# Kernel optimization log

Hardware: AMD Instinct MI355X
Metric: run time of the kernel (lower is better)

Reference implementation:

```python
import jax, jax.numpy as jnp
import numpy as np

B, T, E = 2, 2048, 1024
H = 16
DH = E // H  # 64
DFF = 4 * E
EPS = 1e-5


def _layernorm(x, gamma, beta):
    mu = jnp.mean(x, axis=-1, keepdims=True)
    var = jnp.mean((x - mu) ** 2, axis=-1, keepdims=True)
    return (x - mu) * jax.lax.rsqrt(var + EPS) * gamma + beta


def setup_inputs() -> dict:
    key = jax.random.key(0)
    ks = jax.random.split(key, 16)
    s_e = 1.0 / np.sqrt(E)
    s_f = 1.0 / np.sqrt(DFF)
    return {
        "x": jax.random.normal(ks[0], (B, T, E), jnp.float32),
        # per-head QKV projections, stacked over heads [H, E, DH]
        "Wq": jax.random.normal(ks[1], (H, E, DH), jnp.float32) * s_e,
        "bq": jnp.zeros((H, DH), jnp.float32),
        "Wk": jax.random.normal(ks[2], (H, E, DH), jnp.float32) * s_e,
        "bk": jnp.zeros((H, DH), jnp.float32),
        "Wv": jax.random.normal(ks[3], (H, E, DH), jnp.float32) * s_e,
        "bv": jnp.zeros((H, DH), jnp.float32),
        # output projection
        "Wo": jax.random.normal(ks[4], (E, E), jnp.float32) * s_e,
        "bo": jnp.zeros((E,), jnp.float32),
        # feed-forward
        "W1": jax.random.normal(ks[5], (E, DFF), jnp.float32) * s_e,
        "b1": jnp.zeros((DFF,), jnp.float32),
        "W2": jax.random.normal(ks[6], (DFF, E), jnp.float32) * s_f,
        "b2": jnp.zeros((E,), jnp.float32),
        # layernorms
        "gamma1": jnp.ones((E,), jnp.float32),
        "beta1": jnp.zeros((E,), jnp.float32),
        "gamma2": jnp.ones((E,), jnp.float32),
        "beta2": jnp.zeros((E,), jnp.float32),
    }


def reference(x, Wq, bq, Wk, bk, Wv, bv, Wo, bo, W1, b1, W2, b2,
              gamma1, beta1, gamma2, beta2):
    Bc, Tc, Ec = x.shape
    # --- multi-head causal self-attention (dropout = eval/identity) ---
    xn = _layernorm(x, gamma1, beta1)
    q = jnp.einsum('bte,hed->bhtd', xn, Wq) + bq[:, None, :]
    k = jnp.einsum('bte,hed->bhtd', xn, Wk) + bk[:, None, :]
    v = jnp.einsum('bte,hed->bhtd', xn, Wv) + bv[:, None, :]
    scale = 1.0 / np.sqrt(q.shape[-1])
    scores = jnp.einsum('bhtd,bhsd->bhts', q, k) * scale  # [B,H,T,T]
    causal = jnp.tril(jnp.ones((Tc, Tc), bool))
    scores = jnp.where(causal, scores, jnp.float32(-1e9))
    attn = jax.nn.softmax(scores, axis=-1)
    out = jnp.einsum('bhts,bhsd->bhtd', attn, v)          # [B,H,T,DH]
    out = out.transpose(0, 2, 1, 3).reshape(Bc, Tc, Ec)    # concat heads
    out = out @ Wo + bo
    x = x + out
    # --- feed-forward ---
    xn2 = _layernorm(x, gamma2, beta2)
    h = jax.nn.relu(xn2 @ W1 + b1)
    x = x + (h @ W2 + b2)
    return x
```

## Files before the change

kernel.cpp:

```cpp
#include <hip/hip_runtime.h>
#include <stdint.h>

#define BT    4096
#define EDIM  1024
#define TLEN  2048
#define NH    16
#define DHH   64
#define DFFN  4096

typedef short short8 __attribute__((ext_vector_type(8)));
typedef float f32x4  __attribute__((ext_vector_type(4)));

__device__ __forceinline__ float bf2f(unsigned short u) {
    union { unsigned int i; float f; } c; c.i = ((unsigned int)u) << 16; return c.f;
}
__device__ __forceinline__ unsigned short f2bf(float f) {
    union { float f; unsigned int i; } c; c.f = f;
    unsigned int u = c.i;
    unsigned int r = u + 0x7fffu + ((u >> 16) & 1u);
    return (unsigned short)(r >> 16);
}
__device__ __forceinline__ float fexp2(float x) {
#if __has_builtin(__builtin_amdgcn_exp2f)
    return __builtin_amdgcn_exp2f(x);
#else
    return __expf(x * 0.69314718056f);
#endif
}

template<int QKV>
__global__ __launch_bounds__(256) void transpose_kernel(
    const float* src, unsigned short* dst, int Kdim, int srcStride)
{
    __shared__ float T[64][65];
    int t = threadIdx.x;
    int n0 = blockIdx.x * 64, k0 = blockIdx.y * 64;
    int r = t >> 4, c4 = (t & 15) * 4;
    #pragma unroll
    for (int i = 0; i < 4; i++) {
        int rr = r + i * 16;
        const float* p;
        if (QKV) p = src + ((size_t)(n0 >> 6)) * 65536 + (size_t)(k0 + rr) * 64 + c4;
        else     p = src + (size_t)(k0 + rr) * srcStride + n0 + c4;
        float4 v = *(const float4*)p;
        T[c4 + 0][rr] = v.x;
        T[c4 + 1][rr] = v.y;
        T[c4 + 2][rr] = v.z;
        T[c4 + 3][rr] = v.w;
    }
    __syncthreads();
    int rn = t >> 2, ck = (t & 3) * 16;
    short8 o0, o1;
    #pragma unroll
    for (int j = 0; j < 8; j++) o0[j] = (short)f2bf(T[rn][ck + j]);
    #pragma unroll
    for (int j = 0; j < 8; j++) o1[j] = (short)f2bf(T[rn][ck + 8 + j]);
    unsigned short* dp = dst + (size_t)(n0 + rn) * Kdim + k0 + ck;
    *(short8*)dp       = o0;
    *(short8*)(dp + 8) = o1;
}

__global__ __launch_bounds__(256) void vtrans_kernel(
    const unsigned short* __restrict__ v, unsigned short* __restrict__ vt)
{
    __shared__ __align__(16) unsigned short T[64][72];
    int bh = blockIdx.x, st = blockIdx.y;
    int t = threadIdx.x;
    int r = t >> 2, c = (t & 3) * 16;
    const unsigned short* src = v + ((size_t)bh * TLEN + st * 64) * DHH;
    short8 a0 = *(const short8*)(src + r * DHH + c);
    short8 a1 = *(const short8*)(src + r * DHH + c + 8);
    *(short8*)&T[r][c]     = a0;
    *(short8*)&T[r][c + 8] = a1;
    __syncthreads();
    int d = t >> 2;
    short8 o0, o1;
    #pragma unroll
    for (int j = 0; j < 8; j++) o0[j] = (short)T[c + j][d];
    #pragma unroll
    for (int j = 0; j < 8; j++) o1[j] = (short)T[c + 8 + j][d];
    unsigned short* dst = vt + ((size_t)bh * DHH + d) * TLEN + st * 64 + c;
    *(short8*)dst       = o0;
    *(short8*)(dst + 8) = o1;
}

template<int F32IN>
__global__ __launch_bounds__(256) void ln_stats_kernel(
    const void* __restrict__ x, float* __restrict__ mu_out, float* __restrict__ rstd_out)
{
    int row = blockIdx.x, tid = threadIdx.x;
    size_t off = (size_t)row * EDIM + tid * 4;
    float v0, v1, v2, v3;
    if (F32IN) {
        float4 a = *(const float4*)((const float*)x + off);
        v0 = a.x; v1 = a.y; v2 = a.z; v3 = a.w;
    } else {
        ushort4 raw = *(const ushort4*)((const unsigned short*)x + off);
        v0 = bf2f(raw.x); v1 = bf2f(raw.y); v2 = bf2f(raw.z); v3 = bf2f(raw.w);
    }
    float s  = v0 + v1 + v2 + v3;
    float ss = v0*v0 + v1*v1 + v2*v2 + v3*v3;
    #pragma unroll
    for (int o = 1; o < 64; o <<= 1) {
        s  += __shfl_xor(s,  o, 64);
        ss += __shfl_xor(ss, o, 64);
    }
    __shared__ float red[8];
    int wave = tid >> 6;
    if ((tid & 63) == 0) { red[wave*2] = s; red[wave*2+1] = ss; }
    __syncthreads();
    if (tid == 0) {
        s  = red[0] + red[2] + red[4] + red[6];
        ss = red[1] + red[3] + red[5] + red[7];
        float mu  = s * (1.0f / EDIM);
        float var = ss * (1.0f / EDIM) - mu * mu;
        mu_out[row]   = mu;
        rstd_out[row] = rsqrtf(var + 1e-5f);
    }
}

template<int F32IN>
__global__ __launch_bounds__(256) void ln_apply_kernel(
    const void* __restrict__ x, const float* __restrict__ mu, const float* __restrict__ rstd,
    const float* __restrict__ g, const float* __restrict__ b, unsigned short* __restrict__ out)
{
    int row = blockIdx.x, tid = threadIdx.x;
    float m = mu[row], rs = rstd[row];
    size_t off = (size_t)row * EDIM + tid * 4;
    float v0, v1, v2, v3;
    if (F32IN) {
        float4 a = *(const float4*)((const float*)x + off);
        v0 = a.x; v1 = a.y; v2 = a.z; v3 = a.w;
    } else {
        ushort4 raw = *(const ushort4*)((const unsigned short*)x + off);
        v0 = bf2f(raw.x); v1 = bf2f(raw.y); v2 = bf2f(raw.z); v3 = bf2f(raw.w);
    }
    float4 gv = *(const float4*)(g + tid * 4);
    float4 bv = *(const float4*)(b + tid * 4);
    ushort4 o;
    o.x = f2bf((v0 - m) * rs * gv.x + bv.x);
    o.y = f2bf((v1 - m) * rs * gv.y + bv.y);
    o.z = f2bf((v2 - m) * rs * gv.z + bv.z);
    o.w = f2bf((v3 - m) * rs * gv.w + bv.w);
    *(ushort4*)(out + off) = o;
}

#define V_QKV  0
#define V_WO   1
#define V_FF1  2
#define V_FF2A 3
#define V_FF2B 4
#define LDKK 72

template<int VARIANT, int BN>
__global__ __launch_bounds__(256) void gemm_bt_kernel(
    const unsigned short* A,
    const unsigned short* Bt,
    const float* bias,
    const void* resid,
    void* out,
    int N, int K)
{
    constexpr int NJ = BN / 32;
    __shared__ __align__(16) unsigned short As[128 * LDKK];
    __shared__ __align__(16) unsigned short Bs[BN * LDKK];
    int tid  = threadIdx.x;
    int lane = tid & 63, wave = tid >> 6;
    int quad = lane >> 4, l16 = lane & 15;
    int wr = wave >> 1, wc = wave & 1;
    int m0 = blockIdx.y * 128, n0 = blockIdx.x * BN;

    f32x4 acc[4][NJ];
    #pragma unroll
    for (int i = 0; i < 4; i++)
        #pragma unroll
        for (int j = 0; j < NJ; j++) acc[i][j] = (f32x4){0.f, 0.f, 0.f, 0.f};

    int rowA = tid >> 1, colA = (tid & 1) * 32;
    int rowB, colB;
    if (BN == 128) { rowB = tid >> 1; colB = (tid & 1) * 32; }
    else           { rowB = tid >> 2; colB = (tid & 3) * 16; }

    for (int k0 = 0; k0 < K; k0 += 64) {
        const unsigned short* ap = A + (size_t)(m0 + rowA) * K + k0 + colA;
        short8 a0 = *(const short8*)ap;
        short8 a1 = *(const short8*)(ap + 8);
        short8 a2 = *(const short8*)(ap + 16);
        short8 a3 = *(const short8*)(ap + 24);
        const unsigned short* bp = Bt + (size_t)(n0 + rowB) * K + k0 + colB;
        short8 b0 = *(const short8*)bp;
        short8 b1 = *(const short8*)(bp + 8);
        short8 b2, b3;
        if (BN == 128) {
            b2 = *(const short8*)(bp + 16);
            b3 = *(const short8*)(bp + 24);
        }

        *(short8*)(&As[rowA * LDKK + colA])      = a0;
        *(short8*)(&As[rowA * LDKK + colA + 8])  = a1;
        *(short8*)(&As[rowA * LDKK + colA + 16]) = a2;
        *(short8*)(&As[rowA * LDKK + colA + 24]) = a3;
        *(short8*)(&Bs[rowB * LDKK + colB])      = b0;
        *(short8*)(&Bs[rowB * LDKK + colB + 8])  = b1;
        if (BN == 128) {
            *(short8*)(&Bs[rowB * LDKK + colB + 16]) = b2;
            *(short8*)(&Bs[rowB * LDKK + colB + 24]) = b3;
        }

        __syncthreads();

        #pragma unroll
        for (int ks = 0; ks < 2; ks++) {
            short8 af[4], bf[NJ];
            #pragma unroll
            for (int i = 0; i < 4; i++)
                af[i] = *(const short8*)(&As[(wr * 64 + i * 16 + l16) * LDKK + ks * 32 + quad * 8]);
            #pragma unroll
            for (int j = 0; j < NJ; j++)
                bf[j] = *(const short8*)(&Bs[(wc * (BN / 2) + j * 16 + l16) * LDKK + ks * 32 + quad * 8]);
            #pragma unroll
            for (int i = 0; i < 4; i++)
                #pragma unroll
                for (int j = 0; j < NJ; j++)
                    acc[i][j] = __builtin_amdgcn_mfma_f32_16x16x32_bf16(af[i], bf[j], acc[i][j], 0, 0, 0);
        }

        __syncthreads();
    }

    #pragma unroll
    for (int j = 0; j < NJ; j++) {
        int c = n0 + wc * (BN / 2) + j * 16 + l16;
        float bi = (VARIANT == V_FF2A) ? 0.0f : bias[c];
        #pragma unroll
        for (int i = 0; i < 4; i++) {
            #pragma unroll
            for (int r = 0; r < 4; r++) {
                int m = m0 + wr * 64 + i * 16 + quad * 4 + r;
                float val = acc[i][j][r] + bi;
                if (VARIANT == V_WO)
                    val += ((const float*)resid)[(size_t)m * N + c];
                if (VARIANT == V_FF2B)
                    val += bf2f(((const unsigned short*)resid)[(size_t)m * N + c])
                         + ((const float*)out)[(size_t)m * N + c];
                if (VARIANT == V_FF1)
                    val = fmaxf(val, 0.0f);
                if (VARIANT == V_QKV) {
                    int b = m >> 11, t = m & 2047, h = c >> 6, d = c & 63;
                    ((unsigned short*)out)[(((size_t)(b * NH + h)) * TLEN + t) * DHH + d] = f2bf(val);
                } else if (VARIANT == V_FF2A || VARIANT == V_FF2B) {
                    ((float*)out)[(size_t)m * N + c] = val;
                } else {
                    ((unsigned short*)out)[(size_t)m * N + c] = f2bf(val);
                }
            }
        }
    }
}

__global__ __launch_bounds__(256) void attn_kernel(
    const unsigned short* __restrict__ q,
    const unsigned short* __restrict__ k,
    const unsigned short* __restrict__ vt,
    unsigned short* __restrict__ att)
{
    __shared__ __align__(16) unsigned short Ks[128 * 72];
    __shared__ __align__(16) unsigned short Vs[64 * 136];
    __shared__ __align__(16) unsigned short Ps[4][16 * 136];
    int tid  = threadIdx.x;
    int lane = tid & 63, wave = tid >> 6;
    int quad = lane >> 4, l16 = lane & 15;

    int flat = blockIdx.x;
    int xcd  = flat & 7, idx = flat >> 3;
    int bh   = xcd * 4 + (idx >> 5);
    int qt   = 31 - (idx & 31);
    int q0   = qt * 64;
    int qw   = q0 + wave * 16;

    const unsigned short* Qb = q  + ((size_t)bh * TLEN + qw) * DHH;
    const unsigned short* Kb = k  + (size_t)bh * TLEN * DHH;
    const unsigned short* Vb = vt + (size_t)bh * DHH * TLEN;

    short8 aq0 = *(const short8*)(Qb + l16 * DHH + quad * 8);
    short8 aq1 = *(const short8*)(Qb + l16 * DHH + 32 + quad * 8);

    f32x4 o[4];
    #pragma unroll
    for (int n = 0; n < 4; n++) o[n] = (f32x4){0.f, 0.f, 0.f, 0.f};
    f32x4 mrow = {-1e30f, -1e30f, -1e30f, -1e30f};
    f32x4 lrow = {0.f, 0.f, 0.f, 0.f};
    unsigned short* Pw = Ps[wave];
    const float cs = 0.18033688011f;

    int rowK = tid >> 1, colK = (tid & 1) * 32;
    int rowV = tid >> 2, colV = (tid & 3) * 32;

    int nch = (q0 >> 7) + 1;

    short8 ka0, ka1, ka2, ka3, va0, va1, va2, va3;
    {
        const unsigned short* kp = Kb + (size_t)rowK * DHH + colK;
        ka0 = *(const short8*)kp;
        ka1 = *(const short8*)(kp + 8);
        ka2 = *(const short8*)(kp + 16);
        ka3 = *(const short8*)(kp + 24);
        const unsigned short* vp = Vb + (size_t)rowV * TLEN + colV;
        va0 = *(const short8*)vp;
        va1 = *(const short8*)(vp + 8);
        va2 = *(const short8*)(vp + 16);
        va3 = *(const short8*)(vp + 24);
    }

    for (int ch = 0; ch < nch; ch++) {
        int s0 = ch * 128;
        __syncthreads();
        *(short8*)(&Ks[rowK * 72 + colK])       = ka0;
        *(short8*)(&Ks[rowK * 72 + colK + 8])   = ka1;
        *(short8*)(&Ks[rowK * 72 + colK + 16])  = ka2;
        *(short8*)(&Ks[rowK * 72 + colK + 24])  = ka3;
        *(short8*)(&Vs[rowV * 136 + colV])      = va0;
        *(short8*)(&Vs[rowV * 136 + colV + 8])  = va1;
        *(short8*)(&Vs[rowV * 136 + colV + 16]) = va2;
        *(short8*)(&Vs[rowV * 136 + colV + 24]) = va3;
        __syncthreads();

        if (ch + 1 < nch) {
            int s1 = s0 + 128;
            const unsigned short* kp = Kb + (size_t)(s1 + rowK) * DHH + colK;
            ka0 = *(const short8*)kp;
            ka1 = *(const short8*)(kp + 8);
            ka2 = *(const short8*)(kp + 16);
            ka3 = *(const short8*)(kp + 24);
            const unsigned short* vp = Vb + (size_t)rowV * TLEN + s1 + colV;
            va0 = *(const short8*)vp;
            va1 = *(const short8*)(vp + 8);
            va2 = *(const short8*)(vp + 16);
            va3 = *(const short8*)(vp + 24);
        }

        f32x4 S[8];
        #pragma unroll
        for (int n = 0; n < 8; n++) {
            short8 b0 = *(const short8*)(&Ks[(n * 16 + l16) * 72 + quad * 8]);
            short8 b1 = *(const short8*)(&Ks[(n * 16 + l16) * 72 + 32 + quad * 8]);
            f32x4 s = (f32x4){0.f, 0.f, 0.f, 0.f};
            s = __builtin_amdgcn_mfma_f32_16x16x32_bf16(aq0, b0, s, 0, 0, 0);
            s = __builtin_amdgcn_mfma_f32_16x16x32_bf16(aq1, b1, s, 0, 0, 0);
            S[n] = s;
        }
        bool needmask = (s0 + 127 > qw);
        #pragma unroll
        for (int r = 0; r < 4; r++) {
            float xv[8];
            #pragma unroll
            for (int n = 0; n < 8; n++) {
                float xx = S[n][r] * cs;
                if (needmask && (s0 + n * 16 + l16 > qw + quad * 4 + r)) xx = -1e30f;
                xv[n] = xx;
            }
            float mx = fmaxf(fmaxf(fmaxf(xv[0], xv[1]), fmaxf(xv[2], xv[3])),
                             fmaxf(fmaxf(xv[4], xv[5]), fmaxf(xv[6], xv[7])));
            mx = fmaxf(mx, __shfl_xor(mx, 1, 64));
            mx = fmaxf(mx, __shfl_xor(mx, 2, 64));
            mx = fmaxf(mx, __shfl_xor(mx, 4, 64));
            mx = fmaxf(mx, __shfl_xor(mx, 8, 64));
            float used;
            if (__all(mx <= mrow[r] + 8.0f)) {
                used = mrow[r];
            } else {
                float mnew  = fmaxf(mrow[r], mx);
                float alpha = fexp2(mrow[r] - mnew);
                lrow[r] *= alpha;
                o[0][r] *= alpha; o[1][r] *= alpha;
                o[2][r] *= alpha; o[3][r] *= alpha;
                mrow[r] = mnew;
                used = mnew;
            }
            float ps = 0.f;
            int prow = (quad * 4 + r) * 136;
            #pragma unroll
            for (int n = 0; n < 8; n++) {
                float p = fexp2(xv[n] - used);
                ps += p;
                Pw[prow + n * 16 + l16] = f2bf(p);
            }
            lrow[r] += ps;
        }
        short8 ap[4];
        #pragma unroll
        for (int ks = 0; ks < 4; ks++)
            ap[ks] = *(const short8*)(Pw + l16 * 136 + ks * 32 + quad * 8);
        #pragma unroll
        for (int n = 0; n < 4; n++) {
            #pragma unroll
            for (int ks = 0; ks < 4; ks++) {
                short8 b = *(const short8*)(&Vs[(n * 16 + l16) * 136 + ks * 32 + quad * 8]);
                o[n] = __builtin_amdgcn_mfma_f32_16x16x32_bf16(ap[ks], b, o[n], 0, 0, 0);
            }
        }
    }

    int bidx = bh >> 4, hh = bh & 15;
    #pragma unroll
    for (int r = 0; r < 4; r++) {
        float ls = lrow[r];
        ls += __shfl_xor(ls, 1, 64);
        ls += __shfl_xor(ls, 2, 64);
        ls += __shfl_xor(ls, 4, 64);
        ls += __shfl_xor(ls, 8, 64);
        float inv = 1.0f / ls;
        int t = qw + quad * 4 + r;
        size_t rowoff = ((size_t)(bidx * TLEN + t)) * EDIM + hh * 64;
        #pragma unroll
        for (int n = 0; n < 4; n++)
            att[rowoff + n * 16 + l16] = f2bf(o[n][r] * inv);
    }
}

extern "C" void kernel_launch(void* const* d_in, const int* in_sizes, int n_in,
                              void* d_out, int out_size, void* d_ws, size_t ws_size,
                              hipStream_t stream)
{
    (void)in_sizes; (void)n_in; (void)out_size; (void)ws_size;
    const float* x   = (const float*)d_in[0];
    const float* Wq  = (const float*)d_in[1];
    const float* bq  = (const float*)d_in[2];
    const float* Wk  = (const float*)d_in[3];
    const float* bk  = (const float*)d_in[4];
    const float* Wv  = (const float*)d_in[5];
    const float* bv  = (const float*)d_in[6];
    const float* Wo  = (const float*)d_in[7];
    const float* bo  = (const float*)d_in[8];
    const float* W1  = (const float*)d_in[9];
    const float* b1  = (const float*)d_in[10];
    const float* W2  = (const float*)d_in[11];
    const float* b2  = (const float*)d_in[12];
    const float* g1  = (const float*)d_in[13];
    const float* be1 = (const float*)d_in[14];
    const float* g2  = (const float*)d_in[15];
    const float* be2 = (const float*)d_in[16];

    unsigned short* ws  = (unsigned short*)d_ws;
    unsigned short* xn  = ws;
    unsigned short* vtg = ws;
    unsigned short* qb  = ws + 4194304;
    unsigned short* kb  = ws + 8388608;
    unsigned short* vb  = ws + 12582912;
    unsigned short* wqt = ws + 16777216;
    unsigned short* wkt = ws + 17825792;
    unsigned short* wvt = ws + 18874368;
    unsigned short* att = ws + 16777216;
    unsigned short* x1  = ws + 4194304;
    unsigned short* wot = ws + 8388608;
    unsigned short* w1t = ws + 8388608;
    unsigned short* w2t = ws + 10485760;
    unsigned short* hb  = ws + 12582912;
    float* mu1 = (float*)((char*)d_ws + 41943040);
    float* rs1 = mu1 + 4096;
    float* mu2 = mu1 + 8192;
    float* rs2 = mu1 + 12288;

    dim3 gT64(16, 16);
    dim3 gE(EDIM / 64, BT / 128);
    dim3 gF(2048 / 128, BT / 128);

    transpose_kernel<1><<<gT64, 256, 0, stream>>>(Wq, wqt, EDIM, 64);
    transpose_kernel<1><<<gT64, 256, 0, stream>>>(Wk, wkt, EDIM, 64);
    transpose_kernel<1><<<gT64, 256, 0, stream>>>(Wv, wvt, EDIM, 64);

    ln_stats_kernel<1><<<BT, 256, 0, stream>>>(x, mu1, rs1);
    ln_apply_kernel<1><<<BT, 256, 0, stream>>>(x, mu1, rs1, g1, be1, xn);

    gemm_bt_kernel<V_QKV, 64><<<gE, 256, 0, stream>>>(xn, wqt, bq, nullptr, qb, EDIM, EDIM);
    gemm_bt_kernel<V_QKV, 64><<<gE, 256, 0, stream>>>(xn, wkt, bk, nullptr, kb, EDIM, EDIM);
    gemm_bt_kernel<V_QKV, 64><<<gE, 256, 0, stream>>>(xn, wvt, bv, nullptr, vb, EDIM, EDIM);

    vtrans_kernel<<<dim3(NH * 2, TLEN / 64), 256, 0, stream>>>(vb, vtg);

    attn_kernel<<<dim3(1024), 256, 0, stream>>>(qb, kb, vtg, att);

    transpose_kernel<0><<<gT64, 256, 0, stream>>>(Wo, wot, EDIM, EDIM);
    gemm_bt_kernel<V_WO, 64><<<gE, 256, 0, stream>>>(att, wot, bo, x, x1, EDIM, EDIM);

    ln_stats_kernel<0><<<BT, 256, 0, stream>>>(x1, mu2, rs2);
    ln_apply_kernel<0><<<BT, 256, 0, stream>>>(x1, mu2, rs2, g2, be2, xn);

    transpose_kernel<0><<<dim3(32, 16), 256, 0, stream>>>(W1, w1t, EDIM, DFFN);
    transpose_kernel<0><<<dim3(16, 32), 256, 0, stream>>>(W2, w2t, 2048, EDIM);
    gemm_bt_kernel<V_FF1, 128><<<gF, 256, 0, stream>>>(xn, w1t, b1, nullptr, hb, 2048, EDIM);
    gemm_bt_kernel<V_FF2A, 64><<<gE, 256, 0, stream>>>(hb, w2t, nullptr, nullptr, d_out, EDIM, 2048);
    transpose_kernel<0><<<dim3(32, 16), 256, 0, stream>>>(W1 + 2048, w1t, EDIM, DFFN);
    transpose_kernel<0><<<dim3(16, 32), 256, 0, stream>>>(W2 + (size_t)2048 * EDIM, w2t, 2048, EDIM);
    gemm_bt_kernel<V_FF1, 128><<<gF, 256, 0, stream>>>(xn, w1t, b1 + 2048, nullptr, hb, 2048, EDIM);
    gemm_bt_kernel<V_FF2B, 64><<<gE, 256, 0, stream>>>(hb, w2t, b2, x1, d_out, EDIM, 2048);
}
```

Measured before the change: 463.7 us.

## Use direct global-to-LDS loads in GEMM and fuse Q/K/V projections into one launch

GEMM tile loads now use the global_load_lds builtin, which writes 16-byte chunks straight into unpadded shared memory instead of going through registers. The Q, K and V weight transposes are written contiguously and their biases packed into one buffer, so a single GEMM with N=3072 replaces three launches. The aim is to cut register staging and launch overhead and to fill the GPU better with a larger grid. Dropping the LDS padding can bring back bank conflicts on the MFMA fragment reads.

```diff
diff --git a/kernel.cpp b/kernel.cpp
--- a/kernel.cpp
+++ b/kernel.cpp
@@ -11,6 +11,9 @@
 typedef short short8 __attribute__((ext_vector_type(8)));
 typedef float f32x4  __attribute__((ext_vector_type(4)));
 
+typedef const __attribute__((address_space(1))) unsigned int* gas_ptr;
+typedef __attribute__((address_space(3))) unsigned int*       las_ptr;
+
 __device__ __forceinline__ float bf2f(unsigned short u) {
     union { unsigned int i; float f; } c; c.i = ((unsigned int)u) << 16; return c.f;
 }
@@ -26,6 +29,9 @@
 #else
     return __expf(x * 0.69314718056f);
 #endif
+}
+__device__ __forceinline__ void gload16(const unsigned short* g, unsigned short* l) {
+    __builtin_amdgcn_global_load_lds((gas_ptr)g, (las_ptr)l, 16, 0, 0);
 }
 
 template<int QKV>
@@ -84,6 +90,15 @@
     *(short8*)(dst + 8) = o1;
 }
 
+__global__ __launch_bounds__(256) void bias_fuse_kernel(
+    const float* __restrict__ bq, const float* __restrict__ bk,
+    const float* __restrict__ bv, float* __restrict__ dst)
+{
+    int t = blockIdx.x * 256 + threadIdx.x;
+    const float* src = (t < 1024) ? bq : (t < 2048) ? bk : bv;
+    dst[t] = src[t & 1023];
+}
+
 template<int F32IN>
 __global__ __launch_bounds__(256) void ln_stats_kernel(
     const void* __restrict__ x, float* __restrict__ mu_out, float* __restrict__ rstd_out)
@@ -150,7 +165,6 @@
 #define V_FF1  2
 #define V_FF2A 3
 #define V_FF2B 4
-#define LDKK 72
 
 template<int VARIANT, int BN>
 __global__ __launch_bounds__(256) void gemm_bt_kernel(
@@ -162,8 +176,8 @@
     int N, int K)
 {
     constexpr int NJ = BN / 32;
-    __shared__ __align__(16) unsigned short As[128 * LDKK];
-    __shared__ __align__(16) unsigned short Bs[BN * LDKK];
+    __shared__ __align__(16) unsigned short As[128 * 64];
+    __shared__ __align__(16) unsigned short Bs[BN * 64];
     int tid  = threadIdx.x;
     int lane = tid & 63, wave = tid >> 6;
     int quad = lane >> 4, l16 = lane & 15;
@@ -176,37 +190,20 @@
         #pragma unroll
         for (int j = 0; j < NJ; j++) acc[i][j] = (f32x4){0.f, 0.f, 0.f, 0.f};
 
-    int rowA = tid >> 1, colA = (tid & 1) * 32;
-    int rowB, colB;
-    if (BN == 128) { rowB = tid >> 1; colB = (tid & 1) * 32; }
-    else           { rowB = tid >> 2; colB = (tid & 3) * 16; }
+    int lr = lane >> 3;
+    int lc = (lane & 7) * 8;
 
     for (int k0 = 0; k0 < K; k0 += 64) {
-        const unsigned short* ap = A + (size_t)(m0 + rowA) * K + k0 + colA;
-        short8 a0 = *(const short8*)ap;
-        short8 a1 = *(const short8*)(ap + 8);
-        short8 a2 = *(const short8*)(ap + 16);
-        short8 a3 = *(const short8*)(ap + 24);
-        const unsigned short* bp = Bt + (size_t)(n0 + rowB) * K + k0 + colB;
-        short8 b0 = *(const short8*)bp;
-        short8 b1 = *(const short8*)(bp + 8);
-        short8 b2, b3;
-        if (BN == 128) {
-            b2 = *(const short8*)(bp + 16);
-            b3 = *(const short8*)(bp + 24);
-        }
-
-        *(short8*)(&As[rowA * LDKK + colA])      = a0;
-        *(short8*)(&As[rowA * LDKK + colA + 8])  = a1;
-        *(short8*)(&As[rowA * LDKK + colA + 16]) = a2;
-        *(short8*)(&As[rowA * LDKK + colA + 24]) = a3;
-        *(short8*)(&Bs[rowB * LDKK + colB])      = b0;
-        *(short8*)(&Bs[rowB * LDKK + colB + 8])  = b1;
-        if (BN == 128) {
-            *(short8*)(&Bs[rowB * LDKK + colB + 16]) = b2;
-            *(short8*)(&Bs[rowB * LDKK + colB + 24]) = b3;
-        }
-
+        #pragma unroll
+        for (int i = 0; i < 4; i++) {
+            int r = (i * 4 + wave) * 8 + lr;
+            gload16(A + (size_t)(m0 + r) * K + k0 + lc, &As[(i * 4 + wave) * 512]);
+        }
+        #pragma unroll
+        for (int i = 0; i < NJ; i++) {
+            int r = (i * 4 + wave) * 8 + lr;
+            gload16(Bt + (size_t)(n0 + r) * K + k0 + lc, &Bs[(i * 4 + wave) * 512]);
+        }
         __syncthreads();
 
         #pragma unroll
@@ -214,10 +211,10 @@
             short8 af[4], bf[NJ];
             #pragma unroll
             for (int i = 0; i < 4; i++)
-                af[i] = *(const short8*)(&As[(wr * 64 + i * 16 + l16) * LDKK + ks * 32 + quad * 8]);
+                af[i] = *(const short8*)(&As[(wr * 64 + i * 16 + l16) * 64 + ks * 32 + quad * 8]);
             #pragma unroll
             for (int j = 0; j < NJ; j++)
-                bf[j] = *(const short8*)(&Bs[(wc * (BN / 2) + j * 16 + l16) * LDKK + ks * 32 + quad * 8]);
+                bf[j] = *(const short8*)(&Bs[(wc * (BN / 2) + j * 16 + l16) * 64 + ks * 32 + quad * 8]);
             #pragma unroll
             for (int i = 0; i < 4; i++)
                 #pragma unroll
@@ -246,8 +243,11 @@
                 if (VARIANT == V_FF1)
                     val = fmaxf(val, 0.0f);
                 if (VARIANT == V_QKV) {
-                    int b = m >> 11, t = m & 2047, h = c >> 6, d = c & 63;
-                    ((unsigned short*)out)[(((size_t)(b * NH + h)) * TLEN + t) * DHH + d] = f2bf(val);
+                    int b = m >> 11, t = m & 2047;
+                    int mat = c >> 10, cc = c & 1023;
+                    int h = cc >> 6, d = cc & 63;
+                    ((unsigned short*)out)[(size_t)mat * 4194304 +
+                        (((size_t)(b * NH + h)) * TLEN + t) * DHH + d] = f2bf(val);
                 } else if (VARIANT == V_FF2A || VARIANT == V_FF2B) {
                     ((float*)out)[(size_t)m * N + c] = val;
                 } else {
@@ -448,14 +448,13 @@
     unsigned short* kb  = ws + 8388608;
     unsigned short* vb  = ws + 12582912;
     unsigned short* wqt = ws + 16777216;
-    unsigned short* wkt = ws + 17825792;
-    unsigned short* wvt = ws + 18874368;
     unsigned short* att = ws + 16777216;
     unsigned short* x1  = ws + 4194304;
     unsigned short* wot = ws + 8388608;
     unsigned short* w1t = ws + 8388608;
     unsigned short* w2t = ws + 10485760;
     unsigned short* hb  = ws + 12582912;
+    float* biasf = (float*)(ws + 19922944);
     float* mu1 = (float*)((char*)d_ws + 41943040);
     float* rs1 = mu1 + 4096;
     float* mu2 = mu1 + 8192;
@@ -463,18 +462,18 @@
 
     dim3 gT64(16, 16);
     dim3 gE(EDIM / 64, BT / 128);
+    dim3 gQKV(3072 / 64, BT / 128);
     dim3 gF(2048 / 128, BT / 128);
 
     transpose_kernel<1><<<gT64, 256, 0, stream>>>(Wq, wqt, EDIM, 64);
-    transpose_kernel<1><<<gT64, 256, 0, stream>>>(Wk, wkt, EDIM, 64);
-    transpose_kernel<1><<<gT64, 256, 0, stream>>>(Wv, wvt, EDIM, 64);
+    transpose_kernel<1><<<gT64, 256, 0, stream>>>(Wk, wqt + 1048576, EDIM, 64);
+    transpose_kernel<1><<<gT64, 256, 0, stream>>>(Wv, wqt + 2097152, EDIM, 64);
+    bias_fuse_kernel<<<dim3(12), 256, 0, stream>>>(bq, bk, bv, biasf);
 
     ln_stats_kernel<1><<<BT, 256, 0, stream>>>(x, mu1, rs1);
     ln_apply_kernel<1><<<BT, 256, 0, stream>>>(x, mu1, rs1, g1, be1, xn);
 
-    gemm_bt_kernel<V_QKV, 64><<<gE, 256, 0, stream>>>(xn, wqt, bq, nullptr, qb, EDIM, EDIM);
-    gemm_bt_kernel<V_QKV, 64><<<gE, 256, 0, stream>>>(xn, wkt, bk, nullptr, kb, EDIM, EDIM);
-    gemm_bt_kernel<V_QKV, 64><<<gE, 256, 0, stream>>>(xn, wvt, bv, nullptr, vb, EDIM, EDIM);
+    gemm_bt_kernel<V_QKV, 64><<<gQKV, 256, 0, stream>>>(xn, wqt, biasf, nullptr, qb, 3072, EDIM);
 
     vtrans_kernel<<<dim3(NH * 2, TLEN / 64), 256, 0, stream>>>(vb, vtg);
 
```

Result: faster. 454.1 us (-2.0%).
